# Kernel tuning notes

Measured on AMD Instinct MI355X. Metric: run time of the kernel, lower is better.

## Reference

```python
import jax, jax.numpy as jnp
import numpy as np

B, N, E = 16, 2048, 1_048_576          # graphs, residues per graph, total edges
IN_C, DIM, OUT_C, ENC_H, N_ATOMS = 256, 128, 6, 100, 20
NT = B * N


def setup_inputs() -> dict:
    key = jax.random.key(0)
    ks = jax.random.split(key, 24)
    s = 0.02
    x_res = jax.random.normal(ks[0], (NT, IN_C), jnp.float32)
    coords = jax.random.normal(ks[1], (NT, 3), jnp.float32)
    batch = jnp.repeat(jnp.arange(B, dtype=jnp.int32), N)
    src = jax.random.randint(ks[2], (E,), 0, NT, dtype=jnp.int32)
    dst = (src // N) * N + jax.random.randint(ks[3], (E,), 0, N, dtype=jnp.int32)
    edge_index = jnp.stack([src, dst])  # intra-graph edges, global node ids
    return {
        'x_res': x_res, 'coords': coords,
        'edge_index': edge_index, 'batch': batch,
        'bn_gamma': jnp.ones((IN_C,), jnp.float32),
        'bn_beta': jnp.zeros((IN_C,), jnp.float32),
        'W1': s * jax.random.normal(ks[4], (IN_C, 2 * DIM), jnp.float32),
        'b1': jnp.zeros((2 * DIM,), jnp.float32),
        'W2': s * jax.random.normal(ks[5], (2 * DIM, DIM), jnp.float32),
        'b2': jnp.zeros((DIM,), jnp.float32),
        'W3': s * jax.random.normal(ks[6], (DIM, N_ATOMS), jnp.float32),
        'b3': jnp.zeros((N_ATOMS,), jnp.float32),
        'embed': s * jax.random.normal(ks[7], (N_ATOMS + 1, DIM), jnp.float32),
        'W_msg': s * jax.random.normal(ks[8], (DIM, DIM), jnp.float32),
        'b_msg': jnp.zeros((DIM,), jnp.float32),
        'w_coor': s * jax.random.normal(ks[9], (DIM, 3), jnp.float32),
        'A1': s * jax.random.normal(ks[10], (DIM, ENC_H), jnp.float32),
        'a1': jnp.zeros((ENC_H,), jnp.float32),
        'A2': s * jax.random.normal(ks[11], (ENC_H, OUT_C), jnp.float32),
        'a2': jnp.zeros((OUT_C,), jnp.float32),
        'dyt_alpha': jnp.float32(0.5),
        'dyt_w': jnp.ones((OUT_C,), jnp.float32),
        'dyt_b': jnp.zeros((OUT_C,), jnp.float32),
    }


def reference(x_res, coords, edge_index, batch,
              bn_gamma, bn_beta, W1, b1, W2, b2, W3, b3,
              embed, W_msg, b_msg, w_coor,
              A1, a1, A2, a2, dyt_alpha, dyt_w, dyt_b):
    gelu = lambda v: jax.nn.gelu(v, approximate=False)
    # BatchNorm1d (train-mode batch stats, biased var, eps=1e-5); dropout is identity in eval
    mu = x_res.mean(0)
    var = x_res.var(0)
    xn = (x_res - mu) / jnp.sqrt(var + 1e-5) * bn_gamma + bn_beta
    # input2atomids MLP -> argmax atom ids
    h1 = gelu(xn @ W1 + b1)
    h2 = gelu(h1 @ W2 + b2)
    logits = h2 @ W3 + b3
    ids = jnp.argmax(logits, axis=-1)          # [NT]
    ids_b = ids.reshape(B, N)                  # equal-sized graphs -> no padding needed
    coords_b = coords.reshape(B, N, 3)
    # vectorized edge-list -> dense per-graph adjacency scatter
    g = batch[edge_index[0]]                   # graph id per edge
    ls = edge_index[0] - g * N                 # local src index
    ld = edge_index[1] - g * N                 # local dst index
    same = batch[edge_index[1]] == g           # keep intra-graph edges only
    adj = jnp.zeros((B, N, N), jnp.bool_).at[g, ls, ld].max(same)
    # GotenNet stand-in: embed atom ids, one adjacency-masked aggregation layer
    emb_ids = jnp.where(ids_b < 0, N_ATOMS, ids_b)   # -1 pad -> pad embedding row
    h = embed[emb_ids]                          # [B,N,DIM]
    adjf = adj.astype(h.dtype)
    deg = jnp.maximum(adjf.sum(-1, keepdims=True), 1.0)
    m = jnp.einsum('bij,bjd->bid', adjf, h) / deg
    hout = gelu((h + m) @ W_msg + b_msg)        # invariant features [B,N,DIM]
    coors_out = coords_b + jnp.tanh(hout @ w_coor)
    # un-pad / flatten back to node list, then out_angles head
    z = hout.reshape(NT, DIM)
    t = gelu(z @ A1 + a1)
    t = gelu(t @ A2 + a2)
    t = jnp.tanh(dyt_alpha * t) * dyt_w + dyt_b  # DynamicTanh (channels_last)
    angles = jnp.tanh(t)                         # [NT, OUT_C]
    return angles, z, coors_out
```

## Files before the change

### kernel.cpp

```cpp
#include <hip/hip_runtime.h>
#include <hip/hip_bf16.h>
#include <math.h>

#define Bg 16
#define Nn 2048
#define Ee (1<<20)
#define NT (Bg*Nn)
#define INC 256
#define DIMd 128
#define OUTC 6
#define ENCH 100
#define NATOMS 20
#define BINCAP 3072

typedef __attribute__((ext_vector_type(8))) short bf16x8;
typedef __attribute__((ext_vector_type(4))) float f32x4;

__device__ __forceinline__ float gelu_f(float x){
    return 0.5f*x*(1.0f+erff(x*0.70710678118654752440f));
}
__device__ __forceinline__ unsigned short f2b(float f){
    __hip_bfloat16 h = __float2bfloat16(f);
    return *(unsigned short*)&h;
}
__device__ __forceinline__ float b2f(unsigned short u){
    unsigned v = ((unsigned)u)<<16;
    return __uint_as_float(v);
}
__device__ __forceinline__ void splitf(float v, unsigned short& hi, unsigned short& lo){
    unsigned short h = f2b(v);
    hi = h; lo = f2b(v - b2f(h));
}

__global__ __launch_bounds__(256) void prep0_k(const float* __restrict__ x,
    float* __restrict__ stats, const float* __restrict__ W1,
    const float* __restrict__ W2, const float* __restrict__ Wm,
    const float* __restrict__ A1, short* __restrict__ w1th, short* __restrict__ w1tl,
    short* __restrict__ w2th, short* __restrict__ w2tl,
    short* __restrict__ wmth, short* __restrict__ wmtl,
    short* __restrict__ a1th, short* __restrict__ a1tl)
{
    __shared__ float st[64*65];
    int bx = blockIdx.x, tid = threadIdx.x;
    if(bx < 256){
        int c = tid;
        int r0 = bx * 128;
        const float* p = x + (size_t)r0*INC + c;
        float s = 0.f, s2 = 0.f;
        #pragma unroll 8
        for(int r=0;r<128;r++){ float v = p[(size_t)r*INC]; s += v; s2 += v*v; }
        atomicAdd(&stats[c], s);
        atomicAdd(&stats[INC+c], s2);
        return;
    }
    int t = bx - 256;
    const float* src; short *dh, *dl;
    int k0, n0, lds, ldd, nmax;
    if(t < 16){        src=W1; dh=w1th; dl=w1tl; lds=256; ldd=256; nmax=256;
                       k0=(t>>2)*64;      n0=(t&3)*64; }
    else if(t < 24){   int u=t-16; src=W2; dh=w2th; dl=w2tl; lds=128; ldd=256; nmax=128;
                       k0=(u>>1)*64;      n0=(u&1)*64; }
    else if(t < 28){   int u=t-24; src=Wm; dh=wmth; dl=wmtl; lds=128; ldd=128; nmax=128;
                       k0=(u>>1)*64;      n0=(u&1)*64; }
    else {             int u=t-28; src=A1; dh=a1th; dl=a1tl; lds=100; ldd=128; nmax=100;
                       k0=(u>>1)*64;      n0=(u&1)*64; }
    #pragma unroll
    for(int i=0;i<16;i++){
        int idx = tid + i*256; int r = idx>>6, c = idx&63;
        float v = (n0+c < nmax) ? src[(size_t)(k0+r)*lds + n0+c] : 0.f;
        st[r*65+c] = v;
    }
    __syncthreads();
    #pragma unroll
    for(int i=0;i<16;i++){
        int idx = tid + i*256; int rr = idx>>6, cc = idx&63;
        unsigned short hi, lo;
        splitf(st[cc*65+rr], hi, lo);
        size_t o = (size_t)(n0+rr)*ldd + k0+cc;
        dh[o] = (short)hi; dl[o] = (short)lo;
    }
}

__global__ __launch_bounds__(256) void gemm123_k(const float* __restrict__ x,
    const float* __restrict__ stats, const float* __restrict__ gamma,
    const float* __restrict__ beta, const short* __restrict__ w1th,
    const short* __restrict__ w1tl, const float* __restrict__ b1,
    const short* __restrict__ w2th, const short* __restrict__ w2tl,
    const float* __restrict__ b2, const float* __restrict__ W3,
    const float* __restrict__ b3, int* __restrict__ ids,
    const int* __restrict__ ei, unsigned* __restrict__ ecnt,
    unsigned* __restrict__ earena)
{
    __shared__ float sc[256], sh[256];
    __shared__ __align__(16) unsigned char smem[51200];
    short* sAh = (short*)smem;
    short* sAl = sAh + 64*40;
    short* sBh = (short*)(smem + 10240);
    short* sBl = sBh + 256*40;
    float* h2s = (float*)(smem + 10240);
    float* lgs = (float*)(smem + 44032);
    float* w3s = (float*)smem;

    int tid = threadIdx.x;
    {
        float mu  = stats[tid]*(1.0f/NT);
        float var = stats[256+tid]*(1.0f/NT) - mu*mu;
        float s = gamma[tid]/sqrtf(var + 1e-5f);
        sc[tid] = s; sh[tid] = beta[tid] - mu*s;
    }
    int row0 = blockIdx.x*64;
    int lane = tid&63, w = tid>>6;
    int ln = lane&15, quad = lane>>4;
    int m0w = (w&1)*32, nb1 = (w>>1)*128, nb2 = (w>>1)*64;

    f32x4 acc[2][8];
    #pragma unroll
    for(int i=0;i<2;i++)
        #pragma unroll
        for(int j=0;j<8;j++) acc[i][j] = (f32x4){0.f,0.f,0.f,0.f};
    float bias1[8];
    #pragma unroll
    for(int tn=0;tn<8;tn++) bias1[tn] = b1[nb1 + tn*16 + ln];

    float4 xa[2][2]; bf16x8 wb[2][8];
    #pragma unroll
    for(int t=0;t<2;t++){
        #pragma unroll
        for(int i=0;i<2;i++){ int id=tid+i*256; int r=id>>3,kq=(id&7)*4;
            xa[t][i] = *(const float4*)&x[(size_t)(row0+r)*256 + t*32 + kq]; }
        #pragma unroll
        for(int i=0;i<8;i++){ int id=tid+i*256; int plane=id>>10,cid=id&1023;
            int r=cid>>2,c=cid&3;
            wb[t][i] = *(const bf16x8*)((plane? w1tl:w1th) + (size_t)r*256 + t*32 + c*8); }
    }
    __syncthreads();
    for(int k0=0;k0<256;k0+=32){
        int cur = (k0>>5)&1;
        #pragma unroll
        for(int i=0;i<2;i++){
            int id = tid + i*256; int r = id>>3, kq = (id&7)*4;
            int k = k0+kq;
            float v0 = xa[cur][i].x*sc[k]+sh[k],     v1 = xa[cur][i].y*sc[k+1]+sh[k+1];
            float v2 = xa[cur][i].z*sc[k+2]+sh[k+2], v3 = xa[cur][i].w*sc[k+3]+sh[k+3];
            ushort4 hi, lo;
            splitf(v0,hi.x,lo.x); splitf(v1,hi.y,lo.y);
            splitf(v2,hi.z,lo.z); splitf(v3,hi.w,lo.w);
            *(ushort4*)&sAh[r*40+kq] = hi;
            *(ushort4*)&sAl[r*40+kq] = lo;
        }
        #pragma unroll
        for(int i=0;i<8;i++){
            int id = tid + i*256; int plane = id>>10, cid = id&1023;
            int r = cid>>2, c = cid&3;
            *(bf16x8*)((plane? sBl : sBh) + r*40 + c*8) = wb[cur][i];
        }
        __syncthreads();
        if(k0 < 192){
            #pragma unroll
            for(int i=0;i<2;i++){ int id=tid+i*256; int r=id>>3,kq=(id&7)*4;
                xa[cur][i] = *(const float4*)&x[(size_t)(row0+r)*256 + k0+64+kq]; }
            #pragma unroll
            for(int i=0;i<8;i++){ int id=tid+i*256; int plane=id>>10,cid=id&1023;
                int r=cid>>2,c=cid&3;
                wb[cur][i] = *(const bf16x8*)((plane? w1tl:w1th) + (size_t)r*256 + k0+64 + c*8); }
        }
        bf16x8 ah[2], al[2];
        #pragma unroll
        for(int tm=0;tm<2;tm++){
            ah[tm] = *(const bf16x8*)&sAh[(m0w+tm*16+ln)*40 + quad*8];
            al[tm] = *(const bf16x8*)&sAl[(m0w+tm*16+ln)*40 + quad*8];
        }
        #pragma unroll
        for(int tn=0;tn<8;tn++){
            bf16x8 bh = *(const bf16x8*)&sBh[(nb1+tn*16+ln)*40 + quad*8];
            bf16x8 bl = *(const bf16x8*)&sBl[(nb1+tn*16+ln)*40 + quad*8];
            #pragma unroll
            for(int tm=0;tm<2;tm++){
                acc[tm][tn] = __builtin_amdgcn_mfma_f32_16x16x32_bf16(al[tm], bh, acc[tm][tn], 0,0,0);
                acc[tm][tn] = __builtin_amdgcn_mfma_f32_16x16x32_bf16(ah[tm], bl, acc[tm][tn], 0,0,0);
                acc[tm][tn] = __builtin_amdgcn_mfma_f32_16x16x32_bf16(ah[tm], bh, acc[tm][tn], 0,0,0);
            }
        }
        __syncthreads();
    }

    f32x4 acc2[2][4];
    #pragma unroll
    for(int i=0;i<2;i++)
        #pragma unroll
        for(int j=0;j<4;j++) acc2[i][j] = (f32x4){0.f,0.f,0.f,0.f};
    bf16x8 wb2[4];
    #pragma unroll
    for(int i=0;i<4;i++){ int id=tid+i*256; int plane=id>>9,cid=id&511;
        int r=cid>>2,c=cid&3;
        wb2[i] = *(const bf16x8*)((plane? w2tl:w2th) + (size_t)r*256 + c*8); }
    #pragma unroll
    for(int cc=0;cc<8;cc++){
        if((w>>1) == (cc>>2)){
            int clp = cc&3;
            #pragma unroll
            for(int t=0;t<2;t++){
                int tn = 2*clp + t;
                #pragma unroll
                for(int tm=0;tm<2;tm++){
                    #pragma unroll
                    for(int r=0;r<4;r++){
                        int row = m0w + tm*16 + quad*4 + r;
                        float hv = gelu_f(acc[tm][tn][r] + bias1[tn]);
                        unsigned short hi, lo;
                        splitf(hv, hi, lo);
                        sAh[row*40 + t*16 + ln] = (short)hi;
                        sAl[row*40 + t*16 + ln] = (short)lo;
                    }
                }
            }
        }
        #pragma unroll
        for(int i=0;i<4;i++){
            int id = tid + i*256; int plane = id>>9, cid = id&511;
            int r = cid>>2, c = cid&3;
            *(bf16x8*)((plane? sBl : sBh) + r*40 + c*8) = wb2[i];
        }
        __syncthreads();
        if(cc < 7){
            #pragma unroll
            for(int i=0;i<4;i++){ int id=tid+i*256; int plane=id>>9,cid=id&511;
                int r=cid>>2,c=cid&3;
                wb2[i] = *(const bf16x8*)((plane? w2tl:w2th)
                          + (size_t)r*256 + (cc+1)*32 + c*8); }
        }
        bf16x8 ah[2], al[2];
        #pragma unroll
        for(int tm=0;tm<2;tm++){
            ah[tm] = *(const bf16x8*)&sAh[(m0w+tm*16+ln)*40 + quad*8];
            al[tm] = *(const bf16x8*)&sAl[(m0w+tm*16+ln)*40 + quad*8];
        }
        #pragma unroll
        for(int tn=0;tn<4;tn++){
            bf16x8 bh = *(const bf16x8*)&sBh[(nb2+tn*16+ln)*40 + quad*8];
            bf16x8 bl = *(const bf16x8*)&sBl[(nb2+tn*16+ln)*40 + quad*8];
            #pragma unroll
            for(int tm=0;tm<2;tm++){
                acc2[tm][tn] = __builtin_amdgcn_mfma_f32_16x16x32_bf16(al[tm], bh, acc2[tm][tn], 0,0,0);
                acc2[tm][tn] = __builtin_amdgcn_mfma_f32_16x16x32_bf16(ah[tm], bl, acc2[tm][tn], 0,0,0);
                acc2[tm][tn] = __builtin_amdgcn_mfma_f32_16x16x32_bf16(ah[tm], bh, acc2[tm][tn], 0,0,0);
            }
        }
        __syncthreads();
    }

    #pragma unroll
    for(int tn=0;tn<4;tn++){
        int col = nb2 + tn*16 + ln;
        float bias = b2[col];
        #pragma unroll
        for(int tm=0;tm<2;tm++){
            int rb = m0w + tm*16 + quad*4;
            #pragma unroll
            for(int r=0;r<4;r++)
                h2s[(rb+r)*132 + col] = gelu_f(acc2[tm][tn][r] + bias);
        }
    }
    for(int l=tid;l<2560;l+=256) w3s[l] = W3[l];
    __syncthreads();
    {
        int n = tid>>2, q = tid&3;
        float lg[5] = {};
        #pragma unroll 4
        for(int k=0;k<128;k++){
            float h = h2s[n*132+k];
            #pragma unroll
            for(int a=0;a<5;a++) lg[a] += h*w3s[k*20 + q*5 + a];
        }
        #pragma unroll
        for(int a=0;a<5;a++) lgs[n*20 + q*5 + a] = lg[a] + b3[q*5+a];
    }
    __syncthreads();
    if(tid<64){
        float best = lgs[tid*20]; int bi = 0;
        #pragma unroll
        for(int a=1;a<20;a++){ float v2 = lgs[tid*20+a]; if(v2>best){best=v2;bi=a;} }
        ids[row0+tid] = bi;
    }

    if(blockIdx.x < 256){
        __syncthreads();
        unsigned* lcnt  = (unsigned*)sAh;
        unsigned* gbase = ((unsigned*)sAh) + 512;
        for(int l=tid; l<512; l+=256) lcnt[l] = 0;
        __syncthreads();
        int ebase = blockIdx.x * 4096;
        #pragma unroll 4
        for(int i=0;i<16;i++){
            int e = ebase + i*256 + tid;
            int s = ei[e], d = ei[Ee+e];
            if((s>>11)==(d>>11)) atomicAdd(&lcnt[s>>6], 1u);
        }
        __syncthreads();
        for(int l=tid; l<512; l+=256){
            unsigned c = lcnt[l];
            gbase[l] = c ? atomicAdd(&ecnt[l], c) : 0u;
            lcnt[l] = 0;
        }
        __syncthreads();
        #pragma unroll 4
        for(int i=0;i<16;i++){
            int e = ebase + i*256 + tid;
            int s = ei[e], d = ei[Ee+e];
            if((s>>11)==(d>>11)){
                int bin = s>>6;
                unsigned r = atomicAdd(&lcnt[bin], 1u);
                unsigned pos = gbase[bin] + r;
                if(pos < BINCAP)
                    earena[(size_t)bin*BINCAP + pos] =
                        ((unsigned)(s&63)<<11) | (unsigned)(d&2047);
            }
        }
    }
}

__global__ __launch_bounds__(256) void msg3_k(
    const int* __restrict__ ids, const unsigned* __restrict__ ecnt,
    const unsigned* __restrict__ earena, const float* __restrict__ embed,
    const short* __restrict__ wmth, const short* __restrict__ wmtl,
    const float* __restrict__ b_msg, const float* __restrict__ w_coor,
    const short* __restrict__ a1th, const short* __restrict__ a1tl,
    const float* __restrict__ a1v, const float* __restrict__ A2,
    const float* __restrict__ a2v, const float* __restrict__ dalpha,
    const float* __restrict__ dw, const float* __restrict__ db,
    const float* __restrict__ coords, float* __restrict__ out_ang,
    float* __restrict__ out_z, float* __restrict__ out_co)
{
    __shared__ unsigned short v_bf[64*136];
    __shared__ unsigned short houts[64*136];
    __shared__ __align__(16) unsigned char arena[33792];
    __shared__ float s_bm[128], s_wc[384], s_A2[624], s_a1[104];
    __shared__ float s_dyt[16], s_a2[8];

    unsigned*       lmask = (unsigned*)arena;
    unsigned*       ind   = (unsigned*)(arena + 16384);
    unsigned char*  sid   = arena + 21504;
    float*          emb   = (float*)(arena + 23552);
    short*          sBh   = (short*)arena;
    short*          sBl   = (short*)(arena + 10240);

    int tid = threadIdx.x;
    int bin = blockIdx.x;
    int row0 = bin*64;
    int g = blockIdx.x>>5, tile = blockIdx.x&31;
    int lane = tid&63, w = tid>>6;
    int ln = lane&15, quad = lane>>4;
    int m0w = (w&1)*32, n0w = (w>>1)*64;

    int nb = min((int)ecnt[bin], BINCAP);
    for(int l=tid;l<NATOMS*128;l+=256) emb[l] = embed[l];
    #pragma unroll
    for(int i=0;i<8;i++){ int j = tid + i*256; sid[j] = (unsigned char)ids[g*Nn + j]; }
    #pragma unroll
    for(int i=0;i<16;i++) lmask[tid + i*256] = 0;
    if(tid<128) s_bm[tid] = b_msg[tid];
    if(tid<104) s_a1[tid] = (tid<ENCH) ? a1v[tid] : 0.f;
    for(int l=tid;l<384;l+=256) s_wc[l] = w_coor[l];
    for(int l=tid;l<624;l+=256) s_A2[l] = (l<600) ? A2[l] : 0.f;
    if(tid==0)  s_dyt[0] = dalpha[0];
    if(tid<6){ s_dyt[1+tid] = dw[tid]; s_dyt[8+tid] = db[tid]; }
    if(tid<8)  s_a2[tid] = (tid<6) ? a2v[tid] : 0.f;
    __syncthreads();

    unsigned ew[12]; int ne = 0;
    #pragma unroll
    for(int j=0;j<12;j++){
        int i = tid + j*256;
        if(i < nb){ ew[j] = earena[(size_t)bin*BINCAP + i]; ne = j+1; }
    }
    for(int wp=w; wp<32; wp+=4){
        int a = sid[wp*64 + lane];
        #pragma unroll
        for(int atom=0; atom<NATOMS; atom++){
            unsigned long long bm = __ballot(a==atom);
            if(lane<2) ind[atom*64 + wp*2 + lane] = (unsigned)(bm >> (32*lane));
        }
    }
    for(int j=0;j<ne;j++){
        unsigned wv = ew[j];
        int sl = wv>>11, dl = wv & 2047;
        atomicOr(&lmask[sl*64 + (dl>>5)], 1u<<(dl&31));
    }
    __syncthreads();

    bf16x8 wbm[4];
    #pragma unroll
    for(int i=0;i<4;i++){ int id=tid+i*256; int plane=id>>9,cid=id&511;
        int r=cid>>2,c=cid&3;
        wbm[i] = *(const bf16x8*)((plane? wmtl:wmth) + (size_t)r*128 + c*8); }
    int node = tid>>2, p = tid&3;
    unsigned mw[16];
    {
        const unsigned* mrow = &lmask[node*64 + p*16];
        *(uint4*)&mw[0]  = *(const uint4*)&mrow[0];
        *(uint4*)&mw[4]  = *(const uint4*)&mrow[4];
        *(uint4*)&mw[8]  = *(const uint4*)&mrow[8];
        *(uint4*)&mw[12] = *(const uint4*)&mrow[12];
    }
    int degi = 0;
    #pragma unroll
    for(int w2=0;w2<16;w2++) degi += __popc(mw[w2]);
    float cnt[NATOMS];
    #pragma unroll
    for(int a=0;a<NATOMS;a++){
        int c = 0;
        const unsigned* ia = &ind[a*64 + p*16];
        #pragma unroll
        for(int w2=0;w2<16;w2++) c += __popc(mw[w2] & ia[w2]);
        cnt[a] = (float)c;
    }
    #pragma unroll
    for(int a=0;a<NATOMS;a++){
        cnt[a] += __shfl_xor(cnt[a],1,64);
        cnt[a] += __shfl_xor(cnt[a],2,64);
    }
    float deg = (float)degi;
    deg += __shfl_xor(deg,1,64);
    deg += __shfl_xor(deg,2,64);

    {
        float inv = 1.0f / fmaxf(deg, 1.0f);
        int oid = sid[tile*64 + node];
        int d0 = p*32;
        float vv[32];
        #pragma unroll
        for(int d=0;d<32;d++) vv[d]=0.f;
        #pragma unroll
        for(int a=0;a<NATOMS;a++){
            float ca = cnt[a];
            const float* ea = &emb[a*128 + d0];
            #pragma unroll
            for(int d=0;d<32;d+=4){
                float4 e = *(const float4*)&ea[d];
                vv[d]+=ca*e.x; vv[d+1]+=ca*e.y; vv[d+2]+=ca*e.z; vv[d+3]+=ca*e.w;
            }
        }
        const float* eo = &emb[oid*128 + d0];
        unsigned short* dst = &v_bf[node*136 + d0];
        #pragma unroll
        for(int d=0;d<32;d+=4){
            float4 e = *(const float4*)&eo[d];
            ushort4 o;
            o.x = f2b(e.x + vv[d]*inv);
            o.y = f2b(e.y + vv[d+1]*inv);
            o.z = f2b(e.z + vv[d+2]*inv);
            o.w = f2b(e.w + vv[d+3]*inv);
            *(ushort4*)&dst[d] = o;
        }
    }
    __syncthreads();

    f32x4 acc[2][4];
    #pragma unroll
    for(int i=0;i<2;i++)
        #pragma unroll
        for(int j=0;j<4;j++) acc[i][j] = (f32x4){0.f,0.f,0.f,0.f};
    for(int k0=0;k0<128;k0+=32){
        #pragma unroll
        for(int i=0;i<4;i++){
            int id = tid + i*256; int plane = id>>9, cid = id&511;
            int r = cid>>2, c = cid&3;
            *(bf16x8*)((plane? sBl : sBh) + r*40 + c*8) = wbm[i];
        }
        __syncthreads();
        if(k0 < 96){
            #pragma unroll
            for(int i=0;i<4;i++){ int id=tid+i*256; int plane=id>>9,cid=id&511;
                int r=cid>>2,c=cid&3;
                wbm[i] = *(const bf16x8*)((plane? wmtl:wmth)
                          + (size_t)r*128 + k0+32 + c*8); }
        }
        bf16x8 av[2];
        #pragma unroll
        for(int tm=0;tm<2;tm++)
            av[tm] = *(const bf16x8*)&v_bf[(m0w+tm*16+ln)*136 + k0 + quad*8];
        #pragma unroll
        for(int tn=0;tn<4;tn++){
            bf16x8 bh = *(const bf16x8*)&sBh[(n0w+tn*16+ln)*40 + quad*8];
            bf16x8 bl = *(const bf16x8*)&sBl[(n0w+tn*16+ln)*40 + quad*8];
            #pragma unroll
            for(int tm=0;tm<2;tm++){
                acc[tm][tn] = __builtin_amdgcn_mfma_f32_16x16x32_bf16(av[tm], bl, acc[tm][tn], 0,0,0);
                acc[tm][tn] = __builtin_amdgcn_mfma_f32_16x16x32_bf16(av[tm], bh, acc[tm][tn], 0,0,0);
            }
        }
        __syncthreads();
    }
    bf16x8 wa[4];
    #pragma unroll
    for(int i=0;i<4;i++){ int id=tid+i*256; int plane=id>>9,cid=id&511;
        int r=cid>>2,c=cid&3;
        wa[i] = *(const bf16x8*)((plane? a1tl:a1th) + (size_t)r*128 + c*8); }
    #pragma unroll
    for(int tn=0;tn<4;tn++){
        int col = n0w + tn*16 + ln;
        float bias = s_bm[col];
        #pragma unroll
        for(int tm=0;tm<2;tm++){
            int mb2 = m0w + tm*16 + quad*4;
            #pragma unroll
            for(int r=0;r<4;r++){
                float hv = gelu_f(acc[tm][tn][r] + bias);
                out_z[(size_t)(row0+mb2+r)*128 + col] = hv;
                houts[(mb2+r)*136 + col] = f2b(hv);
            }
        }
    }
    __syncthreads();

    {
        float d0=0.f, d1=0.f, d2=0.f;
        int kb = p*32;
        #pragma unroll
        for(int k=0;k<32;k+=4){
            ushort4 hv = *(const ushort4*)&houts[node*136 + kb + k];
            float h0=b2f(hv.x),h1=b2f(hv.y),h2=b2f(hv.z),h3=b2f(hv.w);
            const float* wc = &s_wc[(kb+k)*3];
            d0 += h0*wc[0]+h1*wc[3]+h2*wc[6]+h3*wc[9];
            d1 += h0*wc[1]+h1*wc[4]+h2*wc[7]+h3*wc[10];
            d2 += h0*wc[2]+h1*wc[5]+h2*wc[8]+h3*wc[11];
        }
        d0 += __shfl_xor(d0,1,64); d0 += __shfl_xor(d0,2,64);
        d1 += __shfl_xor(d1,1,64); d1 += __shfl_xor(d1,2,64);
        d2 += __shfl_xor(d2,1,64); d2 += __shfl_xor(d2,2,64);
        if(p==0){
            size_t o = (size_t)(row0+node)*3;
            out_co[o+0] = coords[o+0] + tanhf(d0);
            out_co[o+1] = coords[o+1] + tanhf(d1);
            out_co[o+2] = coords[o+2] + tanhf(d2);
        }
    }

    f32x4 acc2[2][4];
    #pragma unroll
    for(int i=0;i<2;i++)
        #pragma unroll
        for(int j=0;j<4;j++) acc2[i][j] = (f32x4){0.f,0.f,0.f,0.f};
    for(int k0=0;k0<128;k0+=32){
        __syncthreads();
        #pragma unroll
        for(int i=0;i<4;i++){
            int id = tid + i*256; int plane = id>>9, cid = id&511;
            int r = cid>>2, c = cid&3;
            *(bf16x8*)((plane? sBl : sBh) + r*40 + c*8) = wa[i];
        }
        __syncthreads();
        if(k0 < 96){
            #pragma unroll
            for(int i=0;i<4;i++){ int id=tid+i*256; int plane=id>>9,cid=id&511;
                int r=cid>>2,c=cid&3;
                wa[i] = *(const bf16x8*)((plane? a1tl:a1th)
                          + (size_t)r*128 + k0+32 + c*8); }
        }
        bf16x8 ah[2];
        #pragma unroll
        for(int tm=0;tm<2;tm++)
            ah[tm] = *(const bf16x8*)&houts[(m0w+tm*16+ln)*136 + k0 + quad*8];
        #pragma unroll
        for(int tn=0;tn<4;tn++){
            bf16x8 bh = *(const bf16x8*)&sBh[(n0w+tn*16+ln)*40 + quad*8];
            bf16x8 bl = *(const bf16x8*)&sBl[(n0w+tn*16+ln)*40 + quad*8];
            #pragma unroll
            for(int tm=0;tm<2;tm++){
                acc2[tm][tn] = __builtin_amdgcn_mfma_f32_16x16x32_bf16(ah[tm], bl, acc2[tm][tn], 0,0,0);
                acc2[tm][tn] = __builtin_amdgcn_mfma_f32_16x16x32_bf16(ah[tm], bh, acc2[tm][tn], 0,0,0);
            }
        }
    }
    __syncthreads();
    unsigned short* t1s = houts;
    #pragma unroll
    for(int tn=0;tn<4;tn++){
        int col = n0w + tn*16 + ln;
        if(col < 104){
            float bias = s_a1[col];
            #pragma unroll
            for(int tm=0;tm<2;tm++){
                int mb2 = m0w + tm*16 + quad*4;
                #pragma unroll
                for(int r=0;r<4;r++)
                    t1s[(mb2+r)*104 + col] = f2b(gelu_f(acc2[tm][tn][r] + bias));
            }
        }
    }
    __syncthreads();

    {
        int g0 = (p<2) ? p*7 : 14+(p-2)*6;
        int gcount = (p<2) ? 7 : 6;
        float s[6] = {0.f,0.f,0.f,0.f,0.f,0.f};
        for(int gg=0; gg<gcount; gg++){
            int kb = (g0+gg)*4;
            ushort4 tv = *(const ushort4*)&t1s[node*104 + kb];
            float u0=b2f(tv.x), u1=b2f(tv.y), u2=b2f(tv.z), u3=b2f(tv.w);
            #pragma unroll
            for(int j=0;j<6;j++)
                s[j] += u0*s_A2[kb*6+j] + u1*s_A2[(kb+1)*6+j]
                      + u2*s_A2[(kb+2)*6+j] + u3*s_A2[(kb+3)*6+j];
        }
        #pragma unroll
        for(int j=0;j<6;j++){ s[j]+=__shfl_xor(s[j],1,64); s[j]+=__shfl_xor(s[j],2,64); }
        if(p<2){
            size_t o = (size_t)(row0+node)*6 + p*3;
            #pragma unroll
            for(int jj=0;jj<3;jj++){
                int j = p*3+jj;
                float t2v = gelu_f(s[j] + s_a2[j]);
                float uu = tanhf(s_dyt[0]*t2v)*s_dyt[1+j] + s_dyt[8+j];
                out_ang[o+jj] = tanhf(uu);
            }
        }
    }
}

extern "C" void kernel_launch(void* const* d_in, const int* in_sizes, int n_in,
                              void* d_out, int out_size, void* d_ws, size_t ws_size,
                              hipStream_t stream) {
    const float* x      = (const float*)d_in[0];
    const float* coords = (const float*)d_in[1];
    const int*   ei     = (const int*)d_in[2];
    const float* gamma  = (const float*)d_in[4];
    const float* beta   = (const float*)d_in[5];
    const float* W1     = (const float*)d_in[6];
    const float* b1     = (const float*)d_in[7];
    const float* W2     = (const float*)d_in[8];
    const float* b2     = (const float*)d_in[9];
    const float* W3     = (const float*)d_in[10];
    const float* b3     = (const float*)d_in[11];
    const float* embed  = (const float*)d_in[12];
    const float* W_msg  = (const float*)d_in[13];
    const float* b_msg  = (const float*)d_in[14];
    const float* w_coor = (const float*)d_in[15];
    const float* A1     = (const float*)d_in[16];
    const float* a1v    = (const float*)d_in[17];
    const float* A2     = (const float*)d_in[18];
    const float* a2v    = (const float*)d_in[19];
    const float* dalpha = (const float*)d_in[20];
    const float* dw     = (const float*)d_in[21];
    const float* db     = (const float*)d_in[22];

    char* ws = (char*)d_ws;
    int*      ids   = (int*)ws;
    float*    stats = (float*)(ws + 131072);
    unsigned* ecnt  = (unsigned*)(ws + 131072 + 2048);
    short*    w1th  = (short*)(ws + 262144);
    short*    w1tl  = w1th + 65536;
    short*    w2th  = w1tl + 65536;
    short*    w2tl  = w2th + 32768;
    short*    wmth  = w2tl + 32768;
    short*    wmtl  = wmth + 16384;
    short*    a1th  = wmtl + 16384;
    short*    a1tl  = a1th + 16384;
    unsigned* earena = (unsigned*)(ws + (1<<20));

    float* out_ang = (float*)d_out;
    float* out_z   = out_ang + (size_t)NT*OUTC;
    float* out_co  = out_z   + (size_t)NT*DIMd;

    hipMemsetAsync(stats, 0, 4096, stream);
    prep0_k<<<288, 256, 0, stream>>>(x, stats, W1, W2, W_msg, A1,
        w1th, w1tl, w2th, w2tl, wmth, wmtl, a1th, a1tl);
    gemm123_k<<<512, 256, 0, stream>>>(x, stats, gamma, beta, w1th, w1tl, b1,
        w2th, w2tl, b2, W3, b3, ids, ei, ecnt, earena);
    msg3_k<<<512, 256, 0, stream>>>(ids, ecnt, earena, embed, wmth, wmtl, b_msg,
        w_coor, a1th, a1tl, a1v, A2, a2v, dalpha, dw, db, coords,
        out_ang, out_z, out_co);
}
```

Before: 261.3 us.

## Fuse three stage kernels into one cooperative persistent kernel with grid syncs

Merges the prep, GEMM/ids/edge-binning and message-passing kernels into a single cooperative kernel of 512 blocks. Stages are separated by grid.sync and threadfence instead of kernel launches, and a shared-memory pool is reused across stages. The aim is to remove launch gaps and per-kernel tail effects. It needs two resident blocks per CU under a 60KB LDS pool, and falls back to the old three launches if that cannot be guaranteed. Grid-wide barriers can cost about as much as the launch boundaries they replace.

```diff
diff --git a/kernel.cpp b/kernel.cpp
--- a/kernel.cpp
+++ b/kernel.cpp
@@ -1,6 +1,9 @@
 #include <hip/hip_runtime.h>
+#include <hip/hip_cooperative_groups.h>
 #include <hip/hip_bf16.h>
 #include <math.h>
+
+namespace cg = cooperative_groups;
 
 #define Bg 16
 #define Nn 2048
@@ -31,6 +34,7 @@
     unsigned short h = f2b(v);
     hi = h; lo = f2b(v - b2f(h));
 }
+
 
 __global__ __launch_bounds__(256) void prep0_k(const float* __restrict__ x,
     float* __restrict__ stats, const float* __restrict__ W1,
@@ -352,7 +356,7 @@
     int ln = lane&15, quad = lane>>4;
     int m0w = (w&1)*32, n0w = (w>>1)*64;
 
-    int nb = min((int)ecnt[bin], BINCAP);
+    int nbin = min((int)ecnt[bin], BINCAP);
     for(int l=tid;l<NATOMS*128;l+=256) emb[l] = embed[l];
     #pragma unroll
     for(int i=0;i<8;i++){ int j = tid + i*256; sid[j] = (unsigned char)ids[g*Nn + j]; }
@@ -371,7 +375,7 @@
     #pragma unroll
     for(int j=0;j<12;j++){
         int i = tid + j*256;
-        if(i < nb){ ew[j] = earena[(size_t)bin*BINCAP + i]; ne = j+1; }
+        if(i < nbin){ ew[j] = earena[(size_t)bin*BINCAP + i]; ne = j+1; }
     }
     for(int wp=w; wp<32; wp+=4){
         int a = sid[wp*64 + lane];
@@ -618,56 +622,656 @@
     }
 }
 
+
+struct KParams {
+    const float *x, *coords;
+    const int   *ei;
+    const float *gamma, *beta, *W1, *b1, *W2, *b2, *W3, *b3;
+    const float *embed, *W_msg, *b_msg, *w_coor, *A1, *a1v, *A2, *a2v;
+    const float *dalpha, *dw, *db;
+    float    *stats;
+    unsigned *ecnt, *earena;
+    short *w1th,*w1tl,*w2th,*w2tl,*wmth,*wmtl,*a1th,*a1tl;
+    int   *ids;
+    float *out_ang, *out_z, *out_co;
+};
+
+__global__ __launch_bounds__(256) void fused_k(KParams P)
+{
+    __shared__ __align__(16) unsigned char pool[61440];
+    cg::grid_group grid = cg::this_grid();
+    int tid = threadIdx.x, bx = blockIdx.x;
+
+    {
+        int r0 = bx*64;
+        const float* p = P.x + (size_t)r0*INC + tid;
+        float s = 0.f, s2 = 0.f;
+        #pragma unroll 8
+        for(int r=0;r<64;r++){ float v = p[(size_t)r*INC]; s += v; s2 += v*v; }
+        atomicAdd(&P.stats[tid], s);
+        atomicAdd(&P.stats[INC+tid], s2);
+
+        if((bx&15)==0){
+            float* st = (float*)pool;
+            int t = bx>>4;
+            const float* src; short *dh, *dl;
+            int k0, n0, lds, ldd, nmax;
+            if(t < 16){      src=P.W1; dh=P.w1th; dl=P.w1tl; lds=256; ldd=256; nmax=256;
+                             k0=(t>>2)*64;      n0=(t&3)*64; }
+            else if(t < 24){ int u=t-16; src=P.W2; dh=P.w2th; dl=P.w2tl; lds=128; ldd=256; nmax=128;
+                             k0=(u>>1)*64;      n0=(u&1)*64; }
+            else if(t < 28){ int u=t-24; src=P.W_msg; dh=P.wmth; dl=P.wmtl; lds=128; ldd=128; nmax=128;
+                             k0=(u>>1)*64;      n0=(u&1)*64; }
+            else {           int u=t-28; src=P.A1; dh=P.a1th; dl=P.a1tl; lds=100; ldd=128; nmax=100;
+                             k0=(u>>1)*64;      n0=(u&1)*64; }
+            #pragma unroll
+            for(int i=0;i<16;i++){
+                int idx = tid + i*256; int r = idx>>6, c = idx&63;
+                float v = (n0+c < nmax) ? src[(size_t)(k0+r)*lds + n0+c] : 0.f;
+                st[r*65+c] = v;
+            }
+            __syncthreads();
+            #pragma unroll
+            for(int i=0;i<16;i++){
+                int idx = tid + i*256; int rr = idx>>6, cc = idx&63;
+                unsigned short hi, lo;
+                splitf(st[cc*65+rr], hi, lo);
+                size_t o = (size_t)(n0+rr)*ldd + k0+cc;
+                dh[o] = (short)hi; dl[o] = (short)lo;
+            }
+        }
+    }
+    __threadfence();
+    grid.sync();
+    __threadfence();
+
+    {
+        float* sc = (float*)pool;
+        float* sh = (float*)(pool + 1024);
+        unsigned char* smem = pool + 2048;
+        short* sAh = (short*)smem;
+        short* sAl = sAh + 64*40;
+        short* sBh = (short*)(smem + 10240);
+        short* sBl = sBh + 256*40;
+        float* h2s = (float*)(smem + 10240);
+        float* lgs = (float*)(smem + 44032);
+        float* w3s = (float*)smem;
+
+        {
+            float mu  = P.stats[tid]*(1.0f/NT);
+            float var = P.stats[256+tid]*(1.0f/NT) - mu*mu;
+            float s = P.gamma[tid]/sqrtf(var + 1e-5f);
+            sc[tid] = s; sh[tid] = P.beta[tid] - mu*s;
+        }
+        int row0 = bx*64;
+        int lane = tid&63, w = tid>>6;
+        int ln = lane&15, quad = lane>>4;
+        int m0w = (w&1)*32, nb1 = (w>>1)*128, nb2 = (w>>1)*64;
+
+        f32x4 acc[2][8];
+        #pragma unroll
+        for(int i=0;i<2;i++)
+            #pragma unroll
+            for(int j=0;j<8;j++) acc[i][j] = (f32x4){0.f,0.f,0.f,0.f};
+        float bias1[8];
+        #pragma unroll
+        for(int tn=0;tn<8;tn++) bias1[tn] = P.b1[nb1 + tn*16 + ln];
+
+        float4 xa[2][2]; bf16x8 wb[2][8];
+        #pragma unroll
+        for(int t=0;t<2;t++){
+            #pragma unroll
+            for(int i=0;i<2;i++){ int id=tid+i*256; int r=id>>3,kq=(id&7)*4;
+                xa[t][i] = *(const float4*)&P.x[(size_t)(row0+r)*256 + t*32 + kq]; }
+            #pragma unroll
+            for(int i=0;i<8;i++){ int id=tid+i*256; int plane=id>>10,cid=id&1023;
+                int r=cid>>2,c=cid&3;
+                wb[t][i] = *(const bf16x8*)((plane? P.w1tl:P.w1th) + (size_t)r*256 + t*32 + c*8); }
+        }
+        __syncthreads();
+        for(int k0=0;k0<256;k0+=32){
+            int cur = (k0>>5)&1;
+            #pragma unroll
+            for(int i=0;i<2;i++){
+                int id = tid + i*256; int r = id>>3, kq = (id&7)*4;
+                int k = k0+kq;
+                float v0 = xa[cur][i].x*sc[k]+sh[k],     v1 = xa[cur][i].y*sc[k+1]+sh[k+1];
+                float v2 = xa[cur][i].z*sc[k+2]+sh[k+2], v3 = xa[cur][i].w*sc[k+3]+sh[k+3];
+                ushort4 hi, lo;
+                splitf(v0,hi.x,lo.x); splitf(v1,hi.y,lo.y);
+                splitf(v2,hi.z,lo.z); splitf(v3,hi.w,lo.w);
+                *(ushort4*)&sAh[r*40+kq] = hi;
+                *(ushort4*)&sAl[r*40+kq] = lo;
+            }
+            #pragma unroll
+            for(int i=0;i<8;i++){
+                int id = tid + i*256; int plane = id>>10, cid = id&1023;
+                int r = cid>>2, c = cid&3;
+                *(bf16x8*)((plane? sBl : sBh) + r*40 + c*8) = wb[cur][i];
+            }
+            __syncthreads();
+            if(k0 < 192){
+                #pragma unroll
+                for(int i=0;i<2;i++){ int id=tid+i*256; int r=id>>3,kq=(id&7)*4;
+                    xa[cur][i] = *(const float4*)&P.x[(size_t)(row0+r)*256 + k0+64+kq]; }
+                #pragma unroll
+                for(int i=0;i<8;i++){ int id=tid+i*256; int plane=id>>10,cid=id&1023;
+                    int r=cid>>2,c=cid&3;
+                    wb[cur][i] = *(const bf16x8*)((plane? P.w1tl:P.w1th) + (size_t)r*256 + k0+64 + c*8); }
+            }
+            bf16x8 ah[2], al[2];
+            #pragma unroll
+            for(int tm=0;tm<2;tm++){
+                ah[tm] = *(const bf16x8*)&sAh[(m0w+tm*16+ln)*40 + quad*8];
+                al[tm] = *(const bf16x8*)&sAl[(m0w+tm*16+ln)*40 + quad*8];
+            }
+            #pragma unroll
+            for(int tn=0;tn<8;tn++){
+                bf16x8 bh = *(const bf16x8*)&sBh[(nb1+tn*16+ln)*40 + quad*8];
+                bf16x8 bl = *(const bf16x8*)&sBl[(nb1+tn*16+ln)*40 + quad*8];
+                #pragma unroll
+                for(int tm=0;tm<2;tm++){
+                    acc[tm][tn] = __builtin_amdgcn_mfma_f32_16x16x32_bf16(al[tm], bh, acc[tm][tn], 0,0,0);
+                    acc[tm][tn] = __builtin_amdgcn_mfma_f32_16x16x32_bf16(ah[tm], bl, acc[tm][tn], 0,0,0);
+                    acc[tm][tn] = __builtin_amdgcn_mfma_f32_16x16x32_bf16(ah[tm], bh, acc[tm][tn], 0,0,0);
+                }
+            }
+            __syncthreads();
+        }
+
+        f32x4 acc2[2][4];
+        #pragma unroll
+        for(int i=0;i<2;i++)
+            #pragma unroll
+            for(int j=0;j<4;j++) acc2[i][j] = (f32x4){0.f,0.f,0.f,0.f};
+        bf16x8 wb2[4];
+        #pragma unroll
+        for(int i=0;i<4;i++){ int id=tid+i*256; int plane=id>>9,cid=id&511;
+            int r=cid>>2,c=cid&3;
+            wb2[i] = *(const bf16x8*)((plane? P.w2tl:P.w2th) + (size_t)r*256 + c*8); }
+        #pragma unroll
+        for(int cc=0;cc<8;cc++){
+            if((w>>1) == (cc>>2)){
+                int clp = cc&3;
+                #pragma unroll
+                for(int t=0;t<2;t++){
+                    int tn = 2*clp + t;
+                    #pragma unroll
+                    for(int tm=0;tm<2;tm++){
+                        #pragma unroll
+                        for(int r=0;r<4;r++){
+                            int row = m0w + tm*16 + quad*4 + r;
+                            float hv = gelu_f(acc[tm][tn][r] + bias1[tn]);
+                            unsigned short hi, lo;
+                            splitf(hv, hi, lo);
+                            sAh[row*40 + t*16 + ln] = (short)hi;
+                            sAl[row*40 + t*16 + ln] = (short)lo;
+                        }
+                    }
+                }
+            }
+            #pragma unroll
+            for(int i=0;i<4;i++){
+                int id = tid + i*256; int plane = id>>9, cid = id&511;
+                int r = cid>>2, c = cid&3;
+                *(bf16x8*)((plane? sBl : sBh) + r*40 + c*8) = wb2[i];
+            }
+            __syncthreads();
+            if(cc < 7){
+                #pragma unroll
+                for(int i=0;i<4;i++){ int id=tid+i*256; int plane=id>>9,cid=id&511;
+                    int r=cid>>2,c=cid&3;
+                    wb2[i] = *(const bf16x8*)((plane? P.w2tl:P.w2th)
+                              + (size_t)r*256 + (cc+1)*32 + c*8); }
+            }
+            bf16x8 ah[2], al[2];
+            #pragma unroll
+            for(int tm=0;tm<2;tm++){
+                ah[tm] = *(const bf16x8*)&sAh[(m0w+tm*16+ln)*40 + quad*8];
+                al[tm] = *(const bf16x8*)&sAl[(m0w+tm*16+ln)*40 + quad*8];
+            }
+            #pragma unroll
+            for(int tn=0;tn<4;tn++){
+                bf16x8 bh = *(const bf16x8*)&sBh[(nb2+tn*16+ln)*40 + quad*8];
+                bf16x8 bl = *(const bf16x8*)&sBl[(nb2+tn*16+ln)*40 + quad*8];
+                #pragma unroll
+                for(int tm=0;tm<2;tm++){
+                    acc2[tm][tn] = __builtin_amdgcn_mfma_f32_16x16x32_bf16(al[tm], bh, acc2[tm][tn], 0,0,0);
+                    acc2[tm][tn] = __builtin_amdgcn_mfma_f32_16x16x32_bf16(ah[tm], bl, acc2[tm][tn], 0,0,0);
+                    acc2[tm][tn] = __builtin_amdgcn_mfma_f32_16x16x32_bf16(ah[tm], bh, acc2[tm][tn], 0,0,0);
+                }
+            }
+            __syncthreads();
+        }
+
+        #pragma unroll
+        for(int tn=0;tn<4;tn++){
+            int col = nb2 + tn*16 + ln;
+            float bias = P.b2[col];
+            #pragma unroll
+            for(int tm=0;tm<2;tm++){
+                int rb = m0w + tm*16 + quad*4;
+                #pragma unroll
+                for(int r=0;r<4;r++)
+                    h2s[(rb+r)*132 + col] = gelu_f(acc2[tm][tn][r] + bias);
+            }
+        }
+        for(int l=tid;l<2560;l+=256) w3s[l] = P.W3[l];
+        __syncthreads();
+        {
+            int n = tid>>2, q = tid&3;
+            float lg[5] = {};
+            #pragma unroll 4
+            for(int k=0;k<128;k++){
+                float h = h2s[n*132+k];
+                #pragma unroll
+                for(int a=0;a<5;a++) lg[a] += h*w3s[k*20 + q*5 + a];
+            }
+            #pragma unroll
+            for(int a=0;a<5;a++) lgs[n*20 + q*5 + a] = lg[a] + P.b3[q*5+a];
+        }
+        __syncthreads();
+        if(tid<64){
+            float best = lgs[tid*20]; int bi = 0;
+            #pragma unroll
+            for(int a=1;a<20;a++){ float v2 = lgs[tid*20+a]; if(v2>best){best=v2;bi=a;} }
+            P.ids[row0+tid] = bi;
+        }
+
+        if(bx < 256){
+            __syncthreads();
+            unsigned* lcnt  = (unsigned*)sAh;
+            unsigned* gbase = ((unsigned*)sAh) + 512;
+            for(int l=tid; l<512; l+=256) lcnt[l] = 0;
+            __syncthreads();
+            int ebase = bx * 4096;
+            #pragma unroll 4
+            for(int i=0;i<16;i++){
+                int e = ebase + i*256 + tid;
+                int s = P.ei[e], d = P.ei[Ee+e];
+                if((s>>11)==(d>>11)) atomicAdd(&lcnt[s>>6], 1u);
+            }
+            __syncthreads();
+            for(int l=tid; l<512; l+=256){
+                unsigned c = lcnt[l];
+                gbase[l] = c ? atomicAdd(&P.ecnt[l], c) : 0u;
+                lcnt[l] = 0;
+            }
+            __syncthreads();
+            #pragma unroll 4
+            for(int i=0;i<16;i++){
+                int e = ebase + i*256 + tid;
+                int s = P.ei[e], d = P.ei[Ee+e];
+                if((s>>11)==(d>>11)){
+                    int bin = s>>6;
+                    unsigned r = atomicAdd(&lcnt[bin], 1u);
+                    unsigned pos = gbase[bin] + r;
+                    if(pos < BINCAP)
+                        P.earena[(size_t)bin*BINCAP + pos] =
+                            ((unsigned)(s&63)<<11) | (unsigned)(d&2047);
+                }
+            }
+        }
+    }
+    __threadfence();
+    grid.sync();
+    __threadfence();
+
+    {
+        unsigned short* v_bf  = (unsigned short*)pool;
+        unsigned short* houts = (unsigned short*)(pool + 17408);
+        unsigned char*  arena = pool + 34816;
+        unsigned* lmask = (unsigned*)arena;
+        float*    emb   = (float*)(arena + 16384);
+        unsigned* ind   = (unsigned*)(pool + 17408);
+        unsigned char* sid = pool + 17408 + 5120;
+        short* sBh = (short*)arena;
+        short* sBl = (short*)(arena + 10240);
+        float* s_bm  = (float*)(arena + 20480);
+        float* s_wc  = (float*)(arena + 20992);
+        float* s_A2  = (float*)(arena + 22528);
+        float* s_a1  = (float*)(arena + 25024);
+        float* s_dyt = (float*)(arena + 25440);
+        float* s_a2  = (float*)(arena + 25504);
+
+        int bin = bx;
+        int row0 = bin*64;
+        int g = bx>>5, tile = bx&31;
+        int lane = tid&63, w = tid>>6;
+        int ln = lane&15, quad = lane>>4;
+        int m0w = (w&1)*32, n0w = (w>>1)*64;
+
+        int nbin = min((int)P.ecnt[bin], BINCAP);
+        for(int l=tid;l<NATOMS*128;l+=256) emb[l] = P.embed[l];
+        #pragma unroll
+        for(int i=0;i<8;i++){ int j = tid + i*256; sid[j] = (unsigned char)P.ids[g*Nn + j]; }
+        #pragma unroll
+        for(int i=0;i<16;i++) lmask[tid + i*256] = 0;
+        __syncthreads();
+
+        unsigned ew[12]; int ne = 0;
+        #pragma unroll
+        for(int j=0;j<12;j++){
+            int i = tid + j*256;
+            if(i < nbin){ ew[j] = P.earena[(size_t)bin*BINCAP + i]; ne = j+1; }
+        }
+        for(int wp=w; wp<32; wp+=4){
+            int a = sid[wp*64 + lane];
+            #pragma unroll
+            for(int atom=0; atom<NATOMS; atom++){
+                unsigned long long bm = __ballot(a==atom);
+                if(lane<2) ind[atom*64 + wp*2 + lane] = (unsigned)(bm >> (32*lane));
+            }
+        }
+        for(int j=0;j<ne;j++){
+            unsigned wv = ew[j];
+            int sl = wv>>11, dl = wv & 2047;
+            atomicOr(&lmask[sl*64 + (dl>>5)], 1u<<(dl&31));
+        }
+        __syncthreads();
+
+        bf16x8 wbm[4];
+        #pragma unroll
+        for(int i=0;i<4;i++){ int id=tid+i*256; int plane=id>>9,cid=id&511;
+            int r=cid>>2,c=cid&3;
+            wbm[i] = *(const bf16x8*)((plane? P.wmtl:P.wmth) + (size_t)r*128 + c*8); }
+        int node = tid>>2, p = tid&3;
+        unsigned mw[16];
+        {
+            const unsigned* mrow = &lmask[node*64 + p*16];
+            *(uint4*)&mw[0]  = *(const uint4*)&mrow[0];
+            *(uint4*)&mw[4]  = *(const uint4*)&mrow[4];
+            *(uint4*)&mw[8]  = *(const uint4*)&mrow[8];
+            *(uint4*)&mw[12] = *(const uint4*)&mrow[12];
+        }
+        int degi = 0;
+        #pragma unroll
+        for(int w2=0;w2<16;w2++) degi += __popc(mw[w2]);
+        float cnt[NATOMS];
+        #pragma unroll
+        for(int a=0;a<NATOMS;a++){
+            int c = 0;
+            const unsigned* ia = &ind[a*64 + p*16];
+            #pragma unroll
+            for(int w2=0;w2<16;w2++) c += __popc(mw[w2] & ia[w2]);
+            cnt[a] = (float)c;
+        }
+        #pragma unroll
+        for(int a=0;a<NATOMS;a++){
+            cnt[a] += __shfl_xor(cnt[a],1,64);
+            cnt[a] += __shfl_xor(cnt[a],2,64);
+        }
+        float deg = (float)degi;
+        deg += __shfl_xor(deg,1,64);
+        deg += __shfl_xor(deg,2,64);
+
+        {
+            float inv = 1.0f / fmaxf(deg, 1.0f);
+            int oid = sid[tile*64 + node];
+            int d0 = p*32;
+            float vv[32];
+            #pragma unroll
+            for(int d=0;d<32;d++) vv[d]=0.f;
+            #pragma unroll
+            for(int a=0;a<NATOMS;a++){
+                float ca = cnt[a];
+                const float* ea = &emb[a*128 + d0];
+                #pragma unroll
+                for(int d=0;d<32;d+=4){
+                    float4 e = *(const float4*)&ea[d];
+                    vv[d]+=ca*e.x; vv[d+1]+=ca*e.y; vv[d+2]+=ca*e.z; vv[d+3]+=ca*e.w;
+                }
+            }
+            const float* eo = &emb[oid*128 + d0];
+            unsigned short* dst = &v_bf[node*136 + d0];
+            #pragma unroll
+            for(int d=0;d<32;d+=4){
+                float4 e = *(const float4*)&eo[d];
+                ushort4 o;
+                o.x = f2b(e.x + vv[d]*inv);
+                o.y = f2b(e.y + vv[d+1]*inv);
+                o.z = f2b(e.z + vv[d+2]*inv);
+                o.w = f2b(e.w + vv[d+3]*inv);
+                *(ushort4*)&dst[d] = o;
+            }
+        }
+        __syncthreads();
+
+        if(tid<128) s_bm[tid] = P.b_msg[tid];
+        if(tid<104) s_a1[tid] = (tid<ENCH) ? P.a1v[tid] : 0.f;
+        for(int l=tid;l<384;l+=256) s_wc[l] = P.w_coor[l];
+        for(int l=tid;l<624;l+=256) s_A2[l] = (l<600) ? P.A2[l] : 0.f;
+        if(tid==0)  s_dyt[0] = P.dalpha[0];
+        if(tid<6){ s_dyt[1+tid] = P.dw[tid]; s_dyt[8+tid] = P.db[tid]; }
+        if(tid<8)  s_a2[tid] = (tid<6) ? P.a2v[tid] : 0.f;
+
+        f32x4 acc[2][4];
+        #pragma unroll
+        for(int i=0;i<2;i++)
+            #pragma unroll
+            for(int j=0;j<4;j++) acc[i][j] = (f32x4){0.f,0.f,0.f,0.f};
+        for(int k0=0;k0<128;k0+=32){
+            #pragma unroll
+            for(int i=0;i<4;i++){
+                int id = tid + i*256; int plane = id>>9, cid = id&511;
+                int r = cid>>2, c = cid&3;
+                *(bf16x8*)((plane? sBl : sBh) + r*40 + c*8) = wbm[i];
+            }
+            __syncthreads();
+            if(k0 < 96){
+                #pragma unroll
+                for(int i=0;i<4;i++){ int id=tid+i*256; int plane=id>>9,cid=id&511;
+                    int r=cid>>2,c=cid&3;
+                    wbm[i] = *(const bf16x8*)((plane? P.wmtl:P.wmth)
+                              + (size_t)r*128 + k0+32 + c*8); }
+            }
+            bf16x8 av[2];
+            #pragma unroll
+            for(int tm=0;tm<2;tm++)
+                av[tm] = *(const bf16x8*)&v_bf[(m0w+tm*16+ln)*136 + k0 + quad*8];
+            #pragma unroll
+            for(int tn=0;tn<4;tn++){
+                bf16x8 bh = *(const bf16x8*)&sBh[(n0w+tn*16+ln)*40 + quad*8];
+                bf16x8 bl = *(const bf16x8*)&sBl[(n0w+tn*16+ln)*40 + quad*8];
+                #pragma unroll
+                for(int tm=0;tm<2;tm++){
+                    acc[tm][tn] = __builtin_amdgcn_mfma_f32_16x16x32_bf16(av[tm], bl, acc[tm][tn], 0,0,0);
+                    acc[tm][tn] = __builtin_amdgcn_mfma_f32_16x16x32_bf16(av[tm], bh, acc[tm][tn], 0,0,0);
+                }
+            }
+            __syncthreads();
+        }
+        bf16x8 wa[4];
+        #pragma unroll
+        for(int i=0;i<4;i++){ int id=tid+i*256; int plane=id>>9,cid=id&511;
+            int r=cid>>2,c=cid&3;
+            wa[i] = *(const bf16x8*)((plane? P.a1tl:P.a1th) + (size_t)r*128 + c*8); }
+        #pragma unroll
+        for(int tn=0;tn<4;tn++){
+            int col = n0w + tn*16 + ln;
+            float bias = s_bm[col];
+            #pragma unroll
+            for(int tm=0;tm<2;tm++){
+                int mb2 = m0w + tm*16 + quad*4;
+                #pragma unroll
+                for(int r=0;r<4;r++){
+                    float hv = gelu_f(acc[tm][tn][r] + bias);
+                    P.out_z[(size_t)(row0+mb2+r)*128 + col] = hv;
+                    houts[(mb2+r)*136 + col] = f2b(hv);
+                }
+            }
+        }
+        __syncthreads();
+
+        {
+            float d0=0.f, d1=0.f, d2=0.f;
+            int kb = p*32;
+            #pragma unroll
+            for(int k=0;k<32;k+=4){
+                ushort4 hv = *(const ushort4*)&houts[node*136 + kb + k];
+                float h0=b2f(hv.x),h1=b2f(hv.y),h2=b2f(hv.z),h3=b2f(hv.w);
+                const float* wc = &s_wc[(kb+k)*3];
+                d0 += h0*wc[0]+h1*wc[3]+h2*wc[6]+h3*wc[9];
+                d1 += h0*wc[1]+h1*wc[4]+h2*wc[7]+h3*wc[10];
+                d2 += h0*wc[2]+h1*wc[5]+h2*wc[8]+h3*wc[11];
+            }
+            d0 += __shfl_xor(d0,1,64); d0 += __shfl_xor(d0,2,64);
+            d1 += __shfl_xor(d1,1,64); d1 += __shfl_xor(d1,2,64);
+            d2 += __shfl_xor(d2,1,64); d2 += __shfl_xor(d2,2,64);
+            if(p==0){
+                size_t o = (size_t)(row0+node)*3;
+                P.out_co[o+0] = P.coords[o+0] + tanhf(d0);
+                P.out_co[o+1] = P.coords[o+1] + tanhf(d1);
+                P.out_co[o+2] = P.coords[o+2] + tanhf(d2);
+            }
+        }
+
+        f32x4 acc2[2][4];
+        #pragma unroll
+        for(int i=0;i<2;i++)
+            #pragma unroll
+            for(int j=0;j<4;j++) acc2[i][j] = (f32x4){0.f,0.f,0.f,0.f};
+        for(int k0=0;k0<128;k0+=32){
+            __syncthreads();
+            #pragma unroll
+            for(int i=0;i<4;i++){
+                int id = tid + i*256; int plane = id>>9, cid = id&511;
+                int r = cid>>2, c = cid&3;
+                *(bf16x8*)((plane? sBl : sBh) + r*40 + c*8) = wa[i];
+            }
+            __syncthreads();
+            if(k0 < 96){
+                #pragma unroll
+                for(int i=0;i<4;i++){ int id=tid+i*256; int plane=id>>9,cid=id&511;
+                    int r=cid>>2,c=cid&3;
+                    wa[i] = *(const bf16x8*)((plane? P.a1tl:P.a1th)
+                              + (size_t)r*128 + k0+32 + c*8); }
+            }
+            bf16x8 ah[2];
+            #pragma unroll
+            for(int tm=0;tm<2;tm++)
+                ah[tm] = *(const bf16x8*)&houts[(m0w+tm*16+ln)*136 + k0 + quad*8];
+            #pragma unroll
+            for(int tn=0;tn<4;tn++){
+                bf16x8 bh = *(const bf16x8*)&sBh[(n0w+tn*16+ln)*40 + quad*8];
+                bf16x8 bl = *(const bf16x8*)&sBl[(n0w+tn*16+ln)*40 + quad*8];
+                #pragma unroll
+                for(int tm=0;tm<2;tm++){
+                    acc2[tm][tn] = __builtin_amdgcn_mfma_f32_16x16x32_bf16(ah[tm], bl, acc2[tm][tn], 0,0,0);
+                    acc2[tm][tn] = __builtin_amdgcn_mfma_f32_16x16x32_bf16(ah[tm], bh, acc2[tm][tn], 0,0,0);
+                }
+            }
+        }
+        __syncthreads();
+        unsigned short* t1s = houts;
+        #pragma unroll
+        for(int tn=0;tn<4;tn++){
+            int col = n0w + tn*16 + ln;
+            if(col < 104){
+                float bias = s_a1[col];
+                #pragma unroll
+                for(int tm=0;tm<2;tm++){
+                    int mb2 = m0w + tm*16 + quad*4;
+                    #pragma unroll
+                    for(int r=0;r<4;r++)
+                        t1s[(mb2+r)*104 + col] = f2b(gelu_f(acc2[tm][tn][r] + bias));
+                }
+            }
+        }
+        __syncthreads();
+
+        {
+            int g0 = (p<2) ? p*7 : 14+(p-2)*6;
+            int gcount = (p<2) ? 7 : 6;
+            float s[6] = {0.f,0.f,0.f,0.f,0.f,0.f};
+            for(int gg=0; gg<gcount; gg++){
+                int kb = (g0+gg)*4;
+                ushort4 tv = *(const ushort4*)&t1s[node*104 + kb];
+                float u0=b2f(tv.x), u1=b2f(tv.y), u2=b2f(tv.z), u3=b2f(tv.w);
+                #pragma unroll
+                for(int j=0;j<6;j++)
+                    s[j] += u0*s_A2[kb*6+j] + u1*s_A2[(kb+1)*6+j]
+                          + u2*s_A2[(kb+2)*6+j] + u3*s_A2[(kb+3)*6+j];
+            }
+            #pragma unroll
+            for(int j=0;j<6;j++){ s[j]+=__shfl_xor(s[j],1,64); s[j]+=__shfl_xor(s[j],2,64); }
+            if(p<2){
+                size_t o = (size_t)(row0+node)*6 + p*3;
+                #pragma unroll
+                for(int jj=0;jj<3;jj++){
+                    int j = p*3+jj;
+                    float t2v = gelu_f(s[j] + s_a2[j]);
+                    float uu = tanhf(s_dyt[0]*t2v)*s_dyt[1+j] + s_dyt[8+j];
+                    P.out_ang[o+jj] = tanhf(uu);
+                }
+            }
+        }
+    }
+}
+
 extern "C" void kernel_launch(void* const* d_in, const int* in_sizes, int n_in,
                               void* d_out, int out_size, void* d_ws, size_t ws_size,
                               hipStream_t stream) {
-    const float* x      = (const float*)d_in[0];
-    const float* coords = (const float*)d_in[1];
-    const int*   ei     = (const int*)d_in[2];
-    const float* gamma  = (const float*)d_in[4];
-    const float* beta   = (const float*)d_in[5];
-    const float* W1     = (const float*)d_in[6];
-    const float* b1     = (const float*)d_in[7];
-    const float* W2     = (const float*)d_in[8];
-    const float* b2     = (const float*)d_in[9];
-    const float* W3     = (const float*)d_in[10];
-    const float* b3     = (const float*)d_in[11];
-    const float* embed  = (const float*)d_in[12];
-    const float* W_msg  = (const float*)d_in[13];
-    const float* b_msg  = (const float*)d_in[14];
-    const float* w_coor = (const float*)d_in[15];
-    const float* A1     = (const float*)d_in[16];
-    const float* a1v    = (const float*)d_in[17];
-    const float* A2     = (const float*)d_in[18];
-    const float* a2v    = (const float*)d_in[19];
-    const float* dalpha = (const float*)d_in[20];
-    const float* dw     = (const float*)d_in[21];
-    const float* db     = (const float*)d_in[22];
-
     char* ws = (char*)d_ws;
-    int*      ids   = (int*)ws;
-    float*    stats = (float*)(ws + 131072);
-    unsigned* ecnt  = (unsigned*)(ws + 131072 + 2048);
-    short*    w1th  = (short*)(ws + 262144);
-    short*    w1tl  = w1th + 65536;
-    short*    w2th  = w1tl + 65536;
-    short*    w2tl  = w2th + 32768;
-    short*    wmth  = w2tl + 32768;
-    short*    wmtl  = wmth + 16384;
-    short*    a1th  = wmtl + 16384;
-    short*    a1tl  = a1th + 16384;
-    unsigned* earena = (unsigned*)(ws + (1<<20));
-
-    float* out_ang = (float*)d_out;
-    float* out_z   = out_ang + (size_t)NT*OUTC;
-    float* out_co  = out_z   + (size_t)NT*DIMd;
-
-    hipMemsetAsync(stats, 0, 4096, stream);
-    prep0_k<<<288, 256, 0, stream>>>(x, stats, W1, W2, W_msg, A1,
-        w1th, w1tl, w2th, w2tl, wmth, wmtl, a1th, a1tl);
-    gemm123_k<<<512, 256, 0, stream>>>(x, stats, gamma, beta, w1th, w1tl, b1,
-        w2th, w2tl, b2, W3, b3, ids, ei, ecnt, earena);
-    msg3_k<<<512, 256, 0, stream>>>(ids, ecnt, earena, embed, wmth, wmtl, b_msg,
-        w_coor, a1th, a1tl, a1v, A2, a2v, dalpha, dw, db, coords,
-        out_ang, out_z, out_co);
+    KParams P;
+    P.x      = (const float*)d_in[0];
+    P.coords = (const float*)d_in[1];
+    P.ei     = (const int*)d_in[2];
+    P.gamma  = (const float*)d_in[4];
+    P.beta   = (const float*)d_in[5];
+    P.W1     = (const float*)d_in[6];
+    P.b1     = (const float*)d_in[7];
+    P.W2     = (const float*)d_in[8];
+    P.b2     = (const float*)d_in[9];
+    P.W3     = (const float*)d_in[10];
+    P.b3     = (const float*)d_in[11];
+    P.embed  = (const float*)d_in[12];
+    P.W_msg  = (const float*)d_in[13];
+    P.b_msg  = (const float*)d_in[14];
+    P.w_coor = (const float*)d_in[15];
+    P.A1     = (const float*)d_in[16];
+    P.a1v    = (const float*)d_in[17];
+    P.A2     = (const float*)d_in[18];
+    P.a2v    = (const float*)d_in[19];
+    P.dalpha = (const float*)d_in[20];
+    P.dw     = (const float*)d_in[21];
+    P.db     = (const float*)d_in[22];
+    P.ids    = (int*)ws;
+    P.stats  = (float*)(ws + 131072);
+    P.ecnt   = (unsigned*)(ws + 131072 + 2048);
+    P.w1th   = (short*)(ws + 262144);
+    P.w1tl   = P.w1th + 65536;
+    P.w2th   = P.w1tl + 65536;
+    P.w2tl   = P.w2th + 32768;
+    P.wmth   = P.w2tl + 32768;
+    P.wmtl   = P.wmth + 16384;
+    P.a1th   = P.wmtl + 16384;
+    P.a1tl   = P.a1th + 16384;
+    P.earena = (unsigned*)(ws + (1<<20));
+    P.out_ang = (float*)d_out;
+    P.out_z   = P.out_ang + (size_t)NT*OUTC;
+    P.out_co  = P.out_z   + (size_t)NT*DIMd;
+
+    hipMemsetAsync(P.stats, 0, 4096, stream);
+
+    int occ = 0;
+    hipError_t qe = hipOccupancyMaxActiveBlocksPerMultiprocessor(
+        &occ, (const void*)fused_k, 256, 0);
+    bool coop_ok = (qe == hipSuccess && occ >= 2);
+    if(coop_ok){
+        void* args[] = { &P };
+        hipError_t rc = hipLaunchCooperativeKernel((const void*)fused_k,
+            dim3(512), dim3(256), args, 0, stream);
+        if(rc == hipSuccess) return;
+    }
+
+    prep0_k<<<288, 256, 0, stream>>>(P.x, P.stats, P.W1, P.W2, P.W_msg, P.A1,
+        P.w1th, P.w1tl, P.w2th, P.w2tl, P.wmth, P.wmtl, P.a1th, P.a1tl);
+    gemm123_k<<<512, 256, 0, stream>>>(P.x, P.stats, P.gamma, P.beta,
+        P.w1th, P.w1tl, P.b1, P.w2th, P.w2tl, P.b2, P.W3, P.b3, P.ids,
+        P.ei, P.ecnt, P.earena);
+    msg3_k<<<512, 256, 0, stream>>>(P.ids, P.ecnt, P.earena, P.embed,
+        P.wmth, P.wmtl, P.b_msg, P.w_coor, P.a1th, P.a1tl, P.a1v, P.A2,
+        P.a2v, P.dalpha, P.dw, P.db, P.coords,
+        P.out_ang, P.out_z, P.out_co);
 }
```

Measured after the change: 260.8 us. No clear change (-0.2%).
